# Optimization experiments

Measured on AMD Instinct MI355X. Metric: run time of the kernel, lower is better.

## Reference

```python
import jax, jax.numpy as jnp
import numpy as np

R_MAX = 6.0
NUM_BASIS = 8
TANH_N = 6.0
RECYCLES = 3
N_NODES = 20000
N_EDGES = 640000
ATTR_DIM = 64
LATENT = 64
LN_EPS = 1e-5


def _layer_norm(x, g, b):
    m = x.mean(-1, keepdims=True)
    v = x.var(-1, keepdims=True)
    return (x - m) * jax.lax.rsqrt(v + LN_EPS) * g + b


def setup_inputs() -> dict:
    key = jax.random.key(0)
    ks = jax.random.split(key, 16)
    d1 = 2 * ATTR_DIM + NUM_BASIS  # 136, edge_feature_mlp input
    d2 = LATENT + ATTR_DIM         # 128, attn_mlp input
    d3 = 2 * LATENT                # 128, latent_update_mlp input
    s1 = 1.0 / np.sqrt(d1)
    s2 = 1.0 / np.sqrt(d2)
    s3 = 1.0 / np.sqrt(d3)
    sf = 1.0 / np.sqrt(NUM_BASIS)
    sg = 1.0 / np.sqrt(2 * LATENT)
    return {
        "edge_index": jax.random.randint(ks[0], (2, N_EDGES), 0, N_NODES, dtype=jnp.int64),
        "edge_length": jax.random.uniform(ks[1], (N_EDGES,), minval=0.5, maxval=R_MAX, dtype=jnp.float32),
        "node_attrs": jax.random.normal(ks[2], (N_NODES, ATTR_DIM), dtype=jnp.float32),
        "ln1_g": jnp.ones((d1,), jnp.float32), "ln1_b": jnp.zeros((d1,), jnp.float32),
        "W1": jax.random.normal(ks[3], (d1, LATENT), jnp.float32) * s1,
        "b1": jnp.zeros((LATENT,), jnp.float32),
        "ln2_g": jnp.ones((d2,), jnp.float32), "ln2_b": jnp.zeros((d2,), jnp.float32),
        "W2": jax.random.normal(ks[4], (d2, 1), jnp.float32) * s2,
        "b2": jnp.zeros((1,), jnp.float32),
        "ln3_g": jnp.ones((d3,), jnp.float32), "ln3_b": jnp.zeros((d3,), jnp.float32),
        "W3": jax.random.normal(ks[5], (d3, LATENT), jnp.float32) * s3,
        "b3": jnp.zeros((LATENT,), jnp.float32),
        "film_W1": jax.random.normal(ks[6], (NUM_BASIS, 4 * LATENT), jnp.float32) * sf,  # swiglu: 2*(2*latent)
        "film_W2": jax.random.normal(ks[7], (2 * LATENT, LATENT), jnp.float32) * sg,
        "resnet_p": jnp.zeros((1,), jnp.float32),
    }


def reference(edge_index, edge_length, node_attrs,
              ln1_g, ln1_b, W1, b1,
              ln2_g, ln2_b, W2, b2,
              ln3_g, ln3_b, W3, b3,
              film_W1, film_W2, resnet_p):
    ec = edge_index[0]
    en = edge_index[1]
    num_nodes = node_attrs.shape[0]
    num_edges = edge_index.shape[1]

    # Bessel radial basis * tanh cutoff
    n = jnp.arange(1, NUM_BASIS + 1, dtype=jnp.float32)
    r = edge_length[:, None]
    bessel = jnp.sqrt(2.0 / R_MAX) * jnp.sin(n * jnp.pi * r / R_MAX) / r  # [E, B]
    cutoff = jnp.tanh(1.0 - (edge_length / R_MAX) ** TANH_N) ** 3          # [E]
    rbf = bessel * cutoff[:, None]                                         # [E, B]

    a_c = node_attrs[ec]  # [E, A] gathered center attrs
    a_n = node_attrs[en]  # [E, A] gathered neighbor attrs

    latents = jnp.zeros((num_edges, LATENT), dtype=jnp.float32)
    for _ in range(RECYCLES):  # num_layers=1, recycles=3 -> 3 block applications
        edge_in = jnp.concatenate([a_c, a_n, rbf], axis=-1)            # [E, 136]
        ef = _layer_norm(edge_in, ln1_g, ln1_b) @ W1 + b1              # [E, L]
        attn_in = jnp.concatenate([ef, a_c], axis=-1)                  # [E, 128]
        scores = (_layer_norm(attn_in, ln2_g, ln2_b) @ W2 + b2)[:, 0]  # [E]
        attn = jax.nn.softmax(scores, axis=0)                          # global edge softmax
        pooled = jax.ops.segment_sum(attn[:, None] * ef, ec, num_segments=num_nodes)  # [N, L]
        upd_in = jnp.concatenate([ef, pooled[ec]], axis=-1)            # [E, 2L]
        upd = _layer_norm(upd_in, ln3_g, ln3_b) @ W3 + b3              # [E, L]
        # FiLM gate from rbf: swiglu hidden then sigmoid output, no bias
        h = rbf @ film_W1                                              # [E, 4L]
        a, g = jnp.split(h, 2, axis=-1)
        gate = jax.nn.sigmoid((jax.nn.silu(a) * g) @ film_W2)          # [E, L]
        upd = upd * gate
        uc = jax.nn.sigmoid(resnet_p)                                  # [1]
        c_old = jax.lax.rsqrt(uc * uc + 1.0)
        latents = c_old * latents + (uc * c_old) * upd
    return latents
```

## Files before the change

### kernel.cpp

```cpp
#include <hip/hip_runtime.h>
#include <math.h>

#define KNOTS 1024
#define LNE 1e-5f
#define R0F 0.5f
#define RMAXF 6.0f
#define PAD 96

__device__ __forceinline__ float hermite_(float v0, float m0, float v1, float m1, float t){
  float A = v1 - v0;
  return v0 + t*(m0 + t*((3.f*A - 2.f*m0 - m1) + t*(m0 + m1 - 2.f*A)));
}

__device__ __forceinline__ float wsum64(float v){
#pragma unroll
  for(int m=32;m>=1;m>>=1) v += __shfl_xor(v, m, 64);
  return v;
}

__global__ __launch_bounds__(256) void k_zero(int* cnt, float* sumExp, int N){
  int i = blockIdx.x*256 + threadIdx.x;
  if(i < N) cnt[i] = 0;
  if(i == 0) sumExp[0] = 0.f;
}

__global__ __launch_bounds__(256) void k_weights(
    const float* ln1_g, const float* ln1_b, const float* W1, const float* b1,
    const float* ln2_g, const float* ln2_b, const float* W2, const float* b2,
    const float* ln3_g, const float* ln3_b, const float* W3, const float* b3,
    const float* resnet_p,
    float* W1gA, float* W1gB, float* W1gBot, float* W3gTop, float* W3gBot,
    float* colsum1, float* c1, float* colsum3, float* c3, float* W2g,
    float* cs1w3, float* c1w3, float* BW3, float* misc){
  int tid = threadIdx.x;
  for(int idx=tid; idx<4096; idx+=256){
    int k = idx>>6;
    W1gA[idx]   = ln1_g[k]*W1[idx];
    W1gB[idx]   = ln1_g[64+k]*W1[4096+idx];
    W3gTop[idx] = ln3_g[k]*W3[idx];
    W3gBot[idx] = ln3_g[64+k]*W3[4096+idx];
  }
  for(int idx=tid; idx<512; idx+=256) W1gBot[idx] = ln1_g[128+(idx>>6)]*W1[8192+idx];
  if(tid<128) W2g[tid] = ln2_g[tid]*W2[tid];
  if(tid<64){
    float cs=0.f, cc=0.f;
    for(int k=0;k<136;k++){ float wv = W1[k*64+tid]; cs += ln1_g[k]*wv; cc += ln1_b[k]*wv; }
    colsum1[tid] = cs; c1[tid] = cc + b1[tid];
    float cs3=0.f, cc3=0.f;
    for(int k=0;k<128;k++){ float wv = W3[k*64+tid]; cs3 += ln3_g[k]*wv; cc3 += ln3_b[k]*wv; }
    colsum3[tid] = cs3; c3[tid] = cc3 + b3[tid];
  }
  if(tid==0){
    float cs2=0.f, cc2=0.f;
    for(int k=0;k<128;k++){ cs2 += ln2_g[k]*W2[k]; cc2 += ln2_b[k]*W2[k]; }
    misc[0]=cs2; misc[1]=cc2 + b2[0];
    float p = resnet_p[0];
    float uc = 1.f/(1.f+expf(-p));
    float co = rsqrtf(uc*uc+1.f);
    misc[2] = uc*co*(1.f + co + co*co);
  }
  __syncthreads();
  if(tid<64){
    float a=0.f, b=0.f;
    for(int k=0;k<64;k++){ float wv = W3gTop[k*64+tid]; a += colsum1[k]*wv; b += c1[k]*wv; }
    cs1w3[tid]=a; c1w3[tid]=b;
  }
  for(int idx=tid; idx<512; idx+=256){
    int kk = idx>>6, j = idx&63;
    float a=0.f;
    for(int k=0;k<64;k++) a += W1gBot[kk*64+k]*W3gTop[k*64+j];
    BW3[idx]=a;
  }
  if(tid==0){
    float a=0.f,b=0.f;
    for(int k=0;k<64;k++){ a += colsum1[k]*W2g[k]; b += c1[k]*W2g[k]; }
    misc[3]=a; misc[4]=b;
    float a5=0.f, a6=0.f;
    for(int k=0;k<64;k++){ a5 += colsum1[k]; a6 += c1[k]; }
    misc[5]=a5; misc[6]=a6;
    float gg=0.f, gc=0.f, ccs=0.f;
    for(int k=0;k<64;k++){ float g=colsum1[k], c=c1[k]; gg+=g*g; gc+=g*c; ccs+=c*c; }
    misc[16]=gg; misc[17]=gc; misc[18]=ccs;
  }
  if(tid<8){
    float a=0.f;
    for(int k=0;k<64;k++) a += W1gBot[tid*64+k]*W2g[k];
    misc[8+tid]=a;
  }
}

__device__ __forceinline__ void eval_all(
    float r, const float* W1gBot, const float* BW3, const float* bw2,
    const float* F1, const float* F2, float* uL, int lane, float* rbfO,
    float& T1, float& T13, float& T12, float& gate, float& sr, float& sq){
  float rbf[8];
  float inv_r = 1.f/r;
  float x = r*(1.f/6.f);
  float x2 = x*x;
  float x6 = x2*x2*x2;
  float th = tanhf(1.f - x6);
  float cut = th*th*th;
  float pref = 0.57735026919f*inv_r*cut;
  sr=0.f; sq=0.f;
#pragma unroll
  for(int n=0;n<8;n++){
    float b = pref*sinf((float)(n+1)*0.52359877559f*r);
    rbf[n]=b; rbfO[n]=b; sr+=b; sq+=b*b;
  }
  float t1=0.f,t3=0.f,t2=0.f;
#pragma unroll
  for(int k=0;k<8;k++){
    t1 += rbf[k]*W1gBot[k*64+lane];
    t3 += rbf[k]*BW3[k*64+lane];
    t2 += rbf[k]*bw2[k];
  }
  T1=t1; T13=t3; T12=t2;
  float a0=0.f,a1=0.f,g0=0.f,g1=0.f;
#pragma unroll
  for(int k=0;k<8;k++){
    const float* row = F1 + k*256;
    float rb = rbf[k];
    a0 += rb*row[lane];      a1 += rb*row[64+lane];
    g0 += rb*row[128+lane];  g1 += rb*row[192+lane];
  }
  uL[lane]    = (a0/(1.f+expf(-a0)))*g0;
  uL[64+lane] = (a1/(1.f+expf(-a1)))*g1;
  float accv = 0.f;
  for(int i2=0;i2<128;i2++) accv += uL[i2]*F2[i2*64+lane];
  gate = 1.f/(1.f+expf(-accv));
}

__global__ __launch_bounds__(256) void k_tables(
    const float* W1gBot, const float* BW3, const float* misc,
    const float* F1, const float* F2, const float* colsum1, const float* c1,
    float* tab2, float* tabS, float* tabRbf){
  __shared__ __align__(16) float u[4][128];
  int lane = threadIdx.x&63, w = threadIdx.x>>6;
  int knot = blockIdx.x*4 + w;
  if(knot > KNOTS) return;
  const float H = (RMAXF-R0F)/KNOTS;
  float r = R0F + knot*H;
  const float dh = 1e-3f;
  const float* bw2 = misc+8;
  float rbc[8], rbp[8], rbm[8];
  float T1c,T13c,T12c,Gc,SRc,SQc, T1p,T13p,T12p,Gp,SRp,SQp, T1m,T13m,T12m,Gm,SRm,SQm;
  eval_all(r,    W1gBot,BW3,bw2,F1,F2,u[w],lane, rbc, T1c,T13c,T12c,Gc,SRc,SQc);
  eval_all(r+dh, W1gBot,BW3,bw2,F1,F2,u[w],lane, rbp, T1p,T13p,T12p,Gp,SRp,SQp);
  eval_all(r-dh, W1gBot,BW3,bw2,F1,F2,u[w],lane, rbm, T1m,T13m,T12m,Gm,SRm,SQm);
  float sc = H/(2.f*dh);
  float cg = colsum1[lane], cl = c1[lane];
  float sT1c = wsum64(T1c), sT1p = wsum64(T1p), sT1m = wsum64(T1m);
  float T11c = wsum64(T1c*T1c), T11p = wsum64(T1p*T1p), T11m = wsum64(T1m*T1m);
  float T1gc = wsum64(T1c*cg), T1gp = wsum64(T1p*cg), T1gm = wsum64(T1m*cg);
  float T1cc = wsum64(T1c*cl), T1cp = wsum64(T1p*cl), T1cm = wsum64(T1m*cl);
  ((float4*)tab2)[knot*64+lane] = make_float4(T13c,(T13p-T13m)*sc, Gc,(Gp-Gm)*sc);
  if(lane==0){
    float* d = tabS + knot*16;
    d[0]=SRc;  d[1]=(SRp-SRm)*sc;   d[2]=SQc;  d[3]=(SQp-SQm)*sc;
    d[4]=T12c; d[5]=(T12p-T12m)*sc; d[6]=sT1c; d[7]=(sT1p-sT1m)*sc;
    d[8]=T11c; d[9]=(T11p-T11m)*sc; d[10]=T1gc; d[11]=(T1gp-T1gm)*sc;
    d[12]=T1cc; d[13]=(T1cp-T1cm)*sc; d[14]=0.f; d[15]=0.f;
    float* rb = tabRbf + knot*16;
#pragma unroll
    for(int k=0;k<8;k++){ rb[2*k]=rbc[k]; rb[2*k+1]=(rbp[k]-rbm[k])*sc; }
  }
}

__global__ __launch_bounds__(256) void k_node(
    const float* attrs, const float* W1gA, const float* W1gB, const float* W3gTop,
    const float* W2g, const float* W1gBot, const float* colsum1, const float* c1,
    float* P, float* Q, float* QW3, float* PW3R,
    float* nodeC, float* nodeN, int N){
  __shared__ __align__(16) float sb[4][192];
  int v = (blockIdx.x*256+threadIdx.x)>>6;
  int lane = threadIdx.x&63, w = (threadIdx.x>>6)&3;
  if(v>=N) return;
  const float* av = attrs + (size_t)v*64;
  float al = av[lane];
  sb[w][lane] = al;
  float s = wsum64(al), sqv = wsum64(al*al), t = wsum64(al*W2g[64+lane]);
  float p=0.f, q=0.f;
  const float4* avv = (const float4*)(&sb[w][0]);
#pragma unroll
  for(int kk=0;kk<16;kk++){
    float4 x = avv[kk];
    const float* wa = W1gA + kk*256 + lane;
    const float* wb = W1gB + kk*256 + lane;
    p += x.x*wa[0] + x.y*wa[64] + x.z*wa[128] + x.w*wa[192];
    q += x.x*wb[0] + x.y*wb[64] + x.z*wb[128] + x.w*wb[192];
  }
  P[v*64+lane]=p; Q[v*64+lane]=q;
  float sp = wsum64(p), sq2 = wsum64(q);
  float pw2 = wsum64(p*W2g[lane]), qw2 = wsum64(q*W2g[lane]);
  float cg = colsum1[lane], cl = c1[lane];
  float SPP = wsum64(p*p), SQQ = wsum64(q*q);
  float SPg = wsum64(p*cg), SQg = wsum64(q*cg);
  float SPc = wsum64(p*cl), SQc = wsum64(q*cl);
  float pbv[8], qbv[8];
#pragma unroll
  for(int k=0;k<8;k++){
    float wv = W1gBot[k*64+lane];
    pbv[k] = wsum64(p*wv);
    qbv[k] = wsum64(q*wv);
  }
  sb[w][64+lane]=p; sb[w][128+lane]=q;
  float ap=0.f, aq=0.f;
  const float4* pv = (const float4*)(&sb[w][64]);
  const float4* qv = (const float4*)(&sb[w][128]);
#pragma unroll
  for(int kk=0;kk<16;kk++){
    float4 xp = pv[kk], xq = qv[kk];
    const float* wc = W3gTop + kk*256 + lane;
    ap += xp.x*wc[0] + xp.y*wc[64] + xp.z*wc[128] + xp.w*wc[192];
    aq += xq.x*wc[0] + xq.y*wc[64] + xq.z*wc[128] + xq.w*wc[192];
  }
  PW3R[v*128 + 2*lane] = ap;
  QW3[v*64+lane] = aq;
  if(lane==0){
    float* nc = nodeC + v*16;
    nc[0]=s; nc[1]=sqv; nc[2]=t; nc[3]=pw2; nc[4]=SPP; nc[5]=SPg; nc[6]=SPc; nc[7]=sp;
#pragma unroll
    for(int k=0;k<8;k++) nc[8+k]=pbv[k];
    float* nn = nodeN + v*16;
    nn[0]=s; nn[1]=sqv; nn[2]=sq2; nn[3]=qw2; nn[4]=SQQ; nn[5]=SQg; nn[6]=SQc; nn[7]=0.f;
#pragma unroll
    for(int k=0;k<8;k++) nn[8+k]=qbv[k];
  }
}

__global__ __launch_bounds__(256) void k_bin(const int* ei, const float* elen,
                                             int* cnt, float4* binRec, int N, int E){
  int e = blockIdx.x*256+threadIdx.x;
  if(e<E){
    int c = ei[e]; c = min(max(c,0),N-1);
    int nb = ei[E+e]; nb = min(max(nb,0),N-1);
    float r = elen[e];
    int pos = atomicAdd(&cnt[c],1);
    if(pos < PAD)
      binRec[c*PAD+pos] = make_float4(__int_as_float(nb), r, __int_as_float(e), 0.f);
  }
}

__global__ __launch_bounds__(256) void k_pool(
    const float4* binRec, const int* cnt,
    const float* P, const float* Q,
    const float* nodeC, const float* nodeN, const float* W1gBot,
    const float* colsum1, const float* c1, const float* misc,
    const float* tabS, const float* tabRbf,
    float* pooled, float4* aux, float* sumExp, int N){
  __shared__ float scal[4][PAD][17];
  int w = threadIdx.x>>6, lane = threadIdx.x&63;
  int v = blockIdx.x*4 + w;
  int vv = min(v, N-1);
  int deg = (v<N) ? min(cnt[vv], PAD) : 0;
  const float invH = (float)KNOTS/(RMAXF-R0F);
  int base = vv*PAD;
  {
    float cc0=nodeC[vv*16+0], cc1=nodeC[vv*16+1], cc3=nodeC[vv*16+3];
    float cc4=nodeC[vv*16+4], cc5=nodeC[vv*16+5], cc6=nodeC[vv*16+6], cc7=nodeC[vv*16+7];
    float pb[8];
#pragma unroll
    for(int k=0;k<8;k++) pb[k]=nodeC[vv*16+8+k];
    float csw2=misc[3], cw2=misc[4], sumCol=misc[5], sumC1=misc[6];
    float Sgg=misc[16], Sgc1=misc[17], Sc1c1=misc[18];
    for(int slot=lane; slot<deg; slot+=64){
      float4 rec = binRec[base+slot];
      int nb = __float_as_int(rec.x);
      float r = rec.y;
      float uu = (r-R0F)*invH;
      int ti = (int)uu; ti = min(max(ti,0),KNOTS-1);
      float tt = uu-(float)ti;
      const float4* sA4 = (const float4*)(tabS + ti*16);
      const float4* sB4 = (const float4*)(tabS + (ti+1)*16);
      float4 sA0=sA4[0], sA1=sA4[1], sA2=sA4[2], sA3=sA4[3];
      float4 sB0=sB4[0], sB1=sB4[1], sB2=sB4[2], sB3=sB4[3];
      const float4* rA4 = (const float4*)(tabRbf + ti*16);
      const float4* rB4 = (const float4*)(tabRbf + (ti+1)*16);
      float rbf[8];
      {
        float4 a0=rA4[0], a1=rA4[1], a2=rA4[2], a3=rA4[3];
        float4 b0=rB4[0], b1=rB4[1], b2=rB4[2], b3=rB4[3];
        rbf[0]=hermite_(a0.x,a0.y,b0.x,b0.y,tt); rbf[1]=hermite_(a0.z,a0.w,b0.z,b0.w,tt);
        rbf[2]=hermite_(a1.x,a1.y,b1.x,b1.y,tt); rbf[3]=hermite_(a1.z,a1.w,b1.z,b1.w,tt);
        rbf[4]=hermite_(a2.x,a2.y,b2.x,b2.y,tt); rbf[5]=hermite_(a2.z,a2.w,b2.z,b2.w,tt);
        rbf[6]=hermite_(a3.x,a3.y,b3.x,b3.y,tt); rbf[7]=hermite_(a3.z,a3.w,b3.z,b3.w,tt);
      }
      float srb = hermite_(sA0.x,sA0.y,sB0.x,sB0.y,tt);
      float sqb = hermite_(sA0.z,sA0.w,sB0.z,sB0.w,tt);
      float t1w2= hermite_(sA1.x,sA1.y,sB1.x,sB1.y,tt);
      float sT1 = hermite_(sA1.z,sA1.w,sB1.z,sB1.w,tt);
      float T11 = hermite_(sA2.x,sA2.y,sB2.x,sB2.y,tt);
      float T1g = hermite_(sA2.z,sA2.w,sB2.z,sB2.w,tt);
      float T1c1= hermite_(sA3.x,sA3.y,sB3.x,sB3.y,tt);
      const float4* nn4 = (const float4*)(nodeN + (size_t)nb*16);
      float4 nn0=nn4[0], nn1=nn4[1], nn2=nn4[2], nn3=nn4[3];
      float PT1 = rbf[0]*pb[0]+rbf[1]*pb[1]+rbf[2]*pb[2]+rbf[3]*pb[3]
                + rbf[4]*pb[4]+rbf[5]*pb[5]+rbf[6]*pb[6]+rbf[7]*pb[7];
      float QT1 = rbf[0]*nn2.x+rbf[1]*nn2.y+rbf[2]*nn2.z+rbf[3]*nn2.w
                + rbf[4]*nn3.x+rbf[5]*nn3.y+rbf[6]*nn3.z+rbf[7]*nn3.w;
      float m = (cc0 + nn0.x + srb)*(1.f/136.f);
      float var = (cc1 + nn0.y + sqb)*(1.f/136.f) - m*m;
      float rs = rsqrtf(var + LNE);
      float sumEf = rs*(cc7 + nn0.z + sT1 - m*sumCol) + sumC1;
      float sw = rs*(cc3 + nn0.w + t1w2 - m*csw2) + cw2;
      float SS0 = rs*rs*(cc4 + nn1.x + T11 + 2.f*(PT1+QT1)
                          - 2.f*m*(cc5 + nn1.y + T1g) + m*m*Sgg)
                + 2.f*rs*(cc6 + nn1.z + T1c1 - m*Sgc1) + Sc1c1;
      float* L = &scal[w][slot][0];
      L[0]=rs; L[1]=m; L[2]=sumEf; L[3]=sw; L[4]=SS0; L[5]=2.f*rs*rs;
#pragma unroll
      for(int k=0;k<8;k++) L[6+k]=rbf[k];
    }
  }
  __syncthreads();
  float acc = 0.f, accE = 0.f;
  if(v < N && deg > 0){
    float Pl = P[vv*64+lane];
    float colg1 = colsum1[lane], c1l = c1[lane];
    float w1b[8];
#pragma unroll
    for(int k=0;k<8;k++) w1b[k] = W1gBot[k*64+lane];
    float cc0=nodeC[vv*16+0], cc1=nodeC[vv*16+1], cc2=nodeC[vv*16+2];
    float cs2=misc[0], c2v=misc[1];
    const float inv128 = 1.f/128.f;
    int i1 = min(1, deg-1);
    float4 rA = binRec[base], rB = binRec[base+i1];
    float qA = Q[__float_as_int(rA.x)*64+lane];
    float qB = Q[__float_as_int(rB.x)*64+lane];
    for(int i=0; i<deg; i+=2){
      float4 recA = rA, recB = rB;
      float QlA = qA, QlB = qB;
      bool hasB = (i+1) < deg;
      int iB = min(i+1, deg-1);
      if(i+2 < deg){
        int p0 = i+2, p1 = min(i+3, deg-1);
        rA = binRec[base+p0]; rB = binRec[base+p1];
        qA = Q[__float_as_int(rA.x)*64+lane];
        qB = Q[__float_as_int(rB.x)*64+lane];
      }
      const float* LA = &scal[w][i][0];
      const float* LB = &scal[w][iB][0];
      float rsA=LA[0], mA=LA[1], seA=LA[2], swA=LA[3], S0A=LA[4], cdA=LA[5];
      float rsB=LB[0], mB=LB[1], seB=LB[2], swB=LB[3], S0B=LB[4], cdB=LB[5];
      float T1A = LA[6]*w1b[0]+LA[7]*w1b[1]+LA[8]*w1b[2]+LA[9]*w1b[3]
                + LA[10]*w1b[4]+LA[11]*w1b[5]+LA[12]*w1b[6]+LA[13]*w1b[7];
      float T1B = LB[6]*w1b[0]+LB[7]*w1b[1]+LB[8]*w1b[2]+LB[9]*w1b[3]
                + LB[10]*w1b[4]+LB[11]*w1b[5]+LB[12]*w1b[6]+LB[13]*w1b[7];
      float efA = rsA*(Pl + QlA + T1A - mA*colg1) + c1l;
      float efB = rsB*(Pl + QlB + T1B - mB*colg1) + c1l;
      float dA = Pl*QlA, dB = Pl*QlB;
#pragma unroll
      for(int msk=32; msk>=1; msk>>=1){
        dA += __shfl_xor(dA,msk,64);
        dB += __shfl_xor(dB,msk,64);
      }
      float r1A = S0A + cdA*dA;
      float m2A = (seA + cc0)*inv128;
      float var2A = (r1A + cc1)*inv128 - m2A*m2A;
      float rs2A = rsqrtf(var2A + LNE);
      float scoreA = rs2A*(swA + cc2 - m2A*cs2) + c2v;
      float eevA = __expf(scoreA);
      acc += eevA*efA; accE += eevA;
      if(lane==0) aux[__float_as_int(recA.z)] = make_float4(r1A, rsA, mA, seA);
      if(hasB){
        float r1B = S0B + cdB*dB;
        float m2B = (seB + cc0)*inv128;
        float var2B = (r1B + cc1)*inv128 - m2B*m2B;
        float rs2B = rsqrtf(var2B + LNE);
        float scoreB = rs2B*(swB + cc2 - m2B*cs2) + c2v;
        float eevB = __expf(scoreB);
        acc += eevB*efB; accE += eevB;
        if(lane==0) aux[__float_as_int(recB.z)] = make_float4(r1B, rsB, mB, seB);
      }
    }
  }
  if(v < N){
    pooled[vv*64+lane] = acc;
    if(lane==0 && accE != 0.f) atomicAdd(sumExp, accE);
  }
}

__global__ __launch_bounds__(256) void k_node2(
    const float* pooledRaw, const float* sumExp, const float* W3gBot, const float* nodeC,
    float* PW3R, float4* packF, int N){
  __shared__ __align__(16) float sb[4][64];
  int v = (blockIdx.x*256+threadIdx.x)>>6;
  int lane = threadIdx.x&63, w = (threadIdx.x>>6)&3;
  if(v>=N) return;
  float inv = 1.f/sumExp[0];
  float pl = pooledRaw[v*64+lane]*inv;
  float s = wsum64(pl), sq = wsum64(pl*pl);
  sb[w][lane] = pl;
  float acc = 0.f;
  const float4* pv = (const float4*)(&sb[w][0]);
#pragma unroll
  for(int kk=0;kk<16;kk++){
    float4 x = pv[kk];
    const float* wc = W3gBot + kk*256 + lane;
    acc += x.x*wc[0] + x.y*wc[64] + x.z*wc[128] + x.w*wc[192];
  }
  PW3R[v*128 + 2*lane + 1] = acc;
  if(lane==0){ packF[v] = make_float4(s, sq, nodeC[v*16+7], 0.f); }
}

#define FCHUNK 16
__global__ __launch_bounds__(256) void k_final(
    const int* ei, const float* elen, const float4* aux,
    const float* QW3, const float* PW3R, const float4* packF,
    const float* cs1w3, const float* c1w3, const float* colsum3, const float* c3,
    const float* misc, const float* tab2,
    float* out, int N, int E){
  int w = threadIdx.x>>6, lane = threadIdx.x&63;
  int st = (blockIdx.x*4 + w)*FCHUNK;
  if(st >= E) return;
  int ed = min(st+FCHUNK, E);
  float csw3 = cs1w3[lane], cw3 = c1w3[lane];
  float col3 = colsum3[lane], c3l = c3[lane];
  float SC = misc[2];
  const float invH = (float)KNOTS/(RMAXF-R0F);
  for(int i=st; i<ed; i+=2){
    int eA = i, eB = min(i+1, ed-1);
    int cA = ei[eA];   cA = min(max(cA,0),N-1);
    int nA = ei[E+eA]; nA = min(max(nA,0),N-1);
    int cB = ei[eB];   cB = min(max(cB,0),N-1);
    int nB = ei[E+eB]; nB = min(max(nB,0),N-1);
    float rrA = elen[eA], rrB = elen[eB];
    float4 xA = aux[eA], xB = aux[eB];
    float2 pwA = ((const float2*)PW3R)[cA*64+lane];
    float2 pwB = ((const float2*)PW3R)[cB*64+lane];
    float q3A = QW3[nA*64+lane];
    float q3B = QW3[nB*64+lane];
    float4 pfA = packF[cA], pfB = packF[cB];
    float uuA = (rrA - R0F)*invH;
    int tiA = (int)uuA; tiA = min(max(tiA,0),KNOTS-1);
    float ttA = uuA - (float)tiA;
    int tbA = tiA*64+lane;
    float uuB = (rrB - R0F)*invH;
    int tiB = (int)uuB; tiB = min(max(tiB,0),KNOTS-1);
    float ttB = uuB - (float)tiB;
    int tbB = tiB*64+lane;
    float4 t2aA = ((const float4*)tab2)[tbA], t2bA = ((const float4*)tab2)[tbA+64];
    float4 t2aB = ((const float4*)tab2)[tbB], t2bB = ((const float4*)tab2)[tbB+64];
    {
      float T13 = hermite_(t2aA.x,t2aA.y,t2bA.x,t2bA.y,ttA);
      float gate= hermite_(t2aA.z,t2aA.w,t2bA.z,t2bA.w,ttA);
      float r1 = xA.x, rs = xA.y, m = xA.z, sEf = xA.w;
      float efd = rs*(pwA.x + q3A + T13 - m*csw3) + cw3;
      float m3 = (sEf + pfA.x)*(1.f/128.f);
      float var3 = (r1 + pfA.y)*(1.f/128.f) - m3*m3;
      float rs3 = rsqrtf(var3 + LNE);
      float upd = rs3*(efd + pwA.y - m3*col3) + c3l;
      out[(size_t)eA*64 + lane] = SC*upd*gate;
    }
    {
      float T13 = hermite_(t2aB.x,t2aB.y,t2bB.x,t2bB.y,ttB);
      float gate= hermite_(t2aB.z,t2aB.w,t2bB.z,t2bB.w,ttB);
      float r1 = xB.x, rs = xB.y, m = xB.z, sEf = xB.w;
      float efd = rs*(pwB.x + q3B + T13 - m*csw3) + cw3;
      float m3 = (sEf + pfB.x)*(1.f/128.f);
      float var3 = (r1 + pfB.y)*(1.f/128.f) - m3*m3;
      float rs3 = rsqrtf(var3 + LNE);
      float upd = rs3*(efd + pwB.y - m3*col3) + c3l;
      out[(size_t)eB*64 + lane] = SC*upd*gate;
    }
  }
}

extern "C" void kernel_launch(void* const* d_in, const int* in_sizes, int n_in,
                              void* d_out, int out_size, void* d_ws, size_t ws_size,
                              hipStream_t stream){
  const int*   ei    = (const int*)  d_in[0];
  const float* elen  = (const float*)d_in[1];
  const float* attrs = (const float*)d_in[2];
  const float* ln1_g = (const float*)d_in[3];
  const float* ln1_b = (const float*)d_in[4];
  const float* W1    = (const float*)d_in[5];
  const float* b1    = (const float*)d_in[6];
  const float* ln2_g = (const float*)d_in[7];
  const float* ln2_b = (const float*)d_in[8];
  const float* W2    = (const float*)d_in[9];
  const float* b2    = (const float*)d_in[10];
  const float* ln3_g = (const float*)d_in[11];
  const float* ln3_b = (const float*)d_in[12];
  const float* W3    = (const float*)d_in[13];
  const float* b3    = (const float*)d_in[14];
  const float* F1    = (const float*)d_in[15];
  const float* F2    = (const float*)d_in[16];
  const float* resp  = (const float*)d_in[17];
  const int E = in_sizes[1];
  const int N = in_sizes[2]/64;
  float* ws = (float*)d_ws;
  size_t o = 0;
  auto A = [&](size_t n){ size_t rr = o; o += (n + 63) & ~(size_t)63; return rr; };
  float* P      = ws + A((size_t)N*64);
  float* Q      = ws + A((size_t)N*64);
  float* QW3    = ws + A((size_t)N*64);
  float* PW3R   = ws + A((size_t)N*128);
  float* pooled = ws + A((size_t)N*64);
  float* nodeC  = ws + A((size_t)N*16);
  float* nodeN  = ws + A((size_t)N*16);
  float4* packF = (float4*)(ws + A((size_t)N*4));
  float* W1gA   = ws + A(4096);
  float* W1gB   = ws + A(4096);
  float* W1gBot = ws + A(512);
  float* W3gTop = ws + A(4096);
  float* W3gBot = ws + A(4096);
  float* BW3    = ws + A(512);
  float* colsum1= ws + A(64);
  float* c1     = ws + A(64);
  float* cs1w3  = ws + A(64);
  float* c1w3   = ws + A(64);
  float* colsum3= ws + A(64);
  float* c3     = ws + A(64);
  float* W2g    = ws + A(128);
  float* misc   = ws + A(64);
  float* tab2   = ws + A((size_t)(KNOTS+1)*256);
  float* tabS   = ws + A((size_t)(KNOTS+1)*16);
  float* tabRbf = ws + A((size_t)(KNOTS+1)*16);
  float* sumExp = ws + A(64);
  int* cnt      = (int*)(ws + A((size_t)N));
  float4* binRec= (float4*)(ws + A((size_t)N*PAD*4));
  float4* aux   = (float4*)(ws + A((size_t)E*4));
  (void)ws_size; (void)out_size; (void)n_in;
  float* out = (float*)d_out;

  int nb4 = (N+3)/4;
  k_zero<<<(N+255)/256, 256, 0, stream>>>(cnt, sumExp, N);
  k_weights<<<1,256,0,stream>>>(ln1_g,ln1_b,W1,b1,ln2_g,ln2_b,W2,b2,ln3_g,ln3_b,W3,b3,resp,
      W1gA,W1gB,W1gBot,W3gTop,W3gBot,colsum1,c1,colsum3,c3,W2g,cs1w3,c1w3,BW3,misc);
  k_tables<<<(KNOTS+4)/4, 256, 0, stream>>>(W1gBot,BW3,misc,F1,F2,colsum1,c1,tab2,tabS,tabRbf);
  k_node<<<nb4,256,0,stream>>>(attrs,W1gA,W1gB,W3gTop,W2g,W1gBot,colsum1,c1,P,Q,QW3,PW3R,nodeC,nodeN,N);
  k_bin<<<(E+255)/256,256,0,stream>>>(ei,elen,cnt,binRec,N,E);
  k_pool<<<nb4,256,0,stream>>>(binRec,cnt,P,Q,nodeC,nodeN,W1gBot,colsum1,c1,misc,tabS,tabRbf,pooled,aux,sumExp,N);
  k_node2<<<nb4,256,0,stream>>>(pooled,sumExp,W3gBot,nodeC,PW3R,packF,N);
  {
    int chunks = (E + FCHUNK - 1)/FCHUNK;
    int blocks = (chunks + 3)/4;
    k_final<<<blocks,256,0,stream>>>(ei,elen,aux,QW3,PW3R,packF,cs1w3,c1w3,colsum3,c3,misc,tab2,out,N,E);
  }
}
```

Before: 748.3 us.

## Move attention score computation into per-edge phase and prefetch edge data in final kernel

In k_pool, each lane now computes the full P·Q dot product for its edge from a shared-memory copy of P. It then evaluates the LayerNorm attention score and exp per edge in the first phase, instead of doing a 64-lane shuffle reduction per edge in the serial second loop. The second loop becomes a lean per-edge accumulation over precomputed weights, and the sumExp reduction moves into a wave-level sum. k_final gains software prefetch of edge indices, lengths and aux records for the next pair of edges. The cost is a 64-wide gather of Q per lane in phase one, which adds memory traffic but removes the serialized shuffle chains.

After: 764.1 us. 1.02x slower.

```diff
diff --git a/kernel.cpp b/kernel.cpp
--- a/kernel.cpp
+++ b/kernel.cpp
@@ -248,25 +248,33 @@
     const float* colsum1, const float* c1, const float* misc,
     const float* tabS, const float* tabRbf,
     float* pooled, float4* aux, float* sumExp, int N){
-  __shared__ float scal[4][PAD][17];
+  __shared__ __align__(16) float sP[4][64];
+  __shared__ __align__(16) float scalA[4][PAD][4];
+  __shared__ __align__(16) float scalR[4][PAD][8];
   int w = threadIdx.x>>6, lane = threadIdx.x&63;
   int v = blockIdx.x*4 + w;
   int vv = min(v, N-1);
   int deg = (v<N) ? min(cnt[vv], PAD) : 0;
   const float invH = (float)KNOTS/(RMAXF-R0F);
   int base = vv*PAD;
-  {
-    float cc0=nodeC[vv*16+0], cc1=nodeC[vv*16+1], cc3=nodeC[vv*16+3];
-    float cc4=nodeC[vv*16+4], cc5=nodeC[vv*16+5], cc6=nodeC[vv*16+6], cc7=nodeC[vv*16+7];
+  if(v < N) sP[w][lane] = P[vv*64+lane];
+  __syncthreads();
+  float accE = 0.f;
+  if(v < N){
+    const float* nc = nodeC + vv*16;
+    float cc0=nc[0], cc1=nc[1], cc2=nc[2], cc3=nc[3];
+    float cc4=nc[4], cc5=nc[5], cc6=nc[6], cc7=nc[7];
     float pb[8];
 #pragma unroll
-    for(int k=0;k<8;k++) pb[k]=nodeC[vv*16+8+k];
-    float csw2=misc[3], cw2=misc[4], sumCol=misc[5], sumC1=misc[6];
+    for(int k=0;k<8;k++) pb[k]=nc[8+k];
+    float cs2=misc[0], c2v=misc[1], csw2=misc[3], cw2=misc[4], sumCol=misc[5], sumC1=misc[6];
     float Sgg=misc[16], Sgc1=misc[17], Sc1c1=misc[18];
+    const float4* pp = (const float4*)(&sP[w][0]);
     for(int slot=lane; slot<deg; slot+=64){
       float4 rec = binRec[base+slot];
       int nb = __float_as_int(rec.x);
       float r = rec.y;
+      int orig = __float_as_int(rec.z);
       float uu = (r-R0F)*invH;
       int ti = (int)uu; ti = min(max(ti,0),KNOTS-1);
       float tt = uu-(float)ti;
@@ -294,6 +302,14 @@
       float T1c1= hermite_(sA3.x,sA3.y,sB3.x,sB3.y,tt);
       const float4* nn4 = (const float4*)(nodeN + (size_t)nb*16);
       float4 nn0=nn4[0], nn1=nn4[1], nn2=nn4[2], nn3=nn4[3];
+      const float4* qv4 = (const float4*)(Q + (size_t)nb*64);
+      float dot = 0.f;
+#pragma unroll
+      for(int kk=0;kk<16;kk++){
+        float4 pq = pp[kk];
+        float4 qq = qv4[kk];
+        dot += pq.x*qq.x + pq.y*qq.y + pq.z*qq.z + pq.w*qq.w;
+      }
       float PT1 = rbf[0]*pb[0]+rbf[1]*pb[1]+rbf[2]*pb[2]+rbf[3]*pb[3]
                 + rbf[4]*pb[4]+rbf[5]*pb[5]+rbf[6]*pb[6]+rbf[7]*pb[7];
       float QT1 = rbf[0]*nn2.x+rbf[1]*nn2.y+rbf[2]*nn2.z+rbf[3]*nn2.w
@@ -303,80 +319,50 @@
       float rs = rsqrtf(var + LNE);
       float sumEf = rs*(cc7 + nn0.z + sT1 - m*sumCol) + sumC1;
       float sw = rs*(cc3 + nn0.w + t1w2 - m*csw2) + cw2;
-      float SS0 = rs*rs*(cc4 + nn1.x + T11 + 2.f*(PT1+QT1)
+      float r1 = rs*rs*(cc4 + nn1.x + T11 + 2.f*(PT1+QT1+dot)
                           - 2.f*m*(cc5 + nn1.y + T1g) + m*m*Sgg)
-                + 2.f*rs*(cc6 + nn1.z + T1c1 - m*Sgc1) + Sc1c1;
-      float* L = &scal[w][slot][0];
-      L[0]=rs; L[1]=m; L[2]=sumEf; L[3]=sw; L[4]=SS0; L[5]=2.f*rs*rs;
-#pragma unroll
-      for(int k=0;k<8;k++) L[6+k]=rbf[k];
+               + 2.f*rs*(cc6 + nn1.z + T1c1 - m*Sgc1) + Sc1c1;
+      float m2 = (sumEf + cc0)*(1.f/128.f);
+      float var2 = (r1 + cc1)*(1.f/128.f) - m2*m2;
+      float rs2 = rsqrtf(var2 + LNE);
+      float score = rs2*(sw + cc2 - m2*cs2) + c2v;
+      float eev = __expf(score);
+      accE += eev;
+      aux[orig] = make_float4(r1, rs, m, sumEf);
+      float4* sa = (float4*)&scalA[w][slot][0];
+      *sa = make_float4(eev*rs, eev, m, rec.x);
+      float4* sr4 = (float4*)&scalR[w][slot][0];
+      sr4[0] = make_float4(rbf[0],rbf[1],rbf[2],rbf[3]);
+      sr4[1] = make_float4(rbf[4],rbf[5],rbf[6],rbf[7]);
     }
   }
+  accE = wsum64(accE);
+  if(v < N && lane==0 && accE != 0.f) atomicAdd(sumExp, accE);
   __syncthreads();
-  float acc = 0.f, accE = 0.f;
-  if(v < N && deg > 0){
-    float Pl = P[vv*64+lane];
+  if(v < N){
+    float acc = 0.f;
+    float Pl = sP[w][lane];
     float colg1 = colsum1[lane], c1l = c1[lane];
-    float w1b[8];
-#pragma unroll
-    for(int k=0;k<8;k++) w1b[k] = W1gBot[k*64+lane];
-    float cc0=nodeC[vv*16+0], cc1=nodeC[vv*16+1], cc2=nodeC[vv*16+2];
-    float cs2=misc[0], c2v=misc[1];
-    const float inv128 = 1.f/128.f;
-    int i1 = min(1, deg-1);
-    float4 rA = binRec[base], rB = binRec[base+i1];
-    float qA = Q[__float_as_int(rA.x)*64+lane];
-    float qB = Q[__float_as_int(rB.x)*64+lane];
-    for(int i=0; i<deg; i+=2){
-      float4 recA = rA, recB = rB;
-      float QlA = qA, QlB = qB;
-      bool hasB = (i+1) < deg;
-      int iB = min(i+1, deg-1);
-      if(i+2 < deg){
-        int p0 = i+2, p1 = min(i+3, deg-1);
-        rA = binRec[base+p0]; rB = binRec[base+p1];
-        qA = Q[__float_as_int(rA.x)*64+lane];
-        qB = Q[__float_as_int(rB.x)*64+lane];
-      }
-      const float* LA = &scal[w][i][0];
-      const float* LB = &scal[w][iB][0];
-      float rsA=LA[0], mA=LA[1], seA=LA[2], swA=LA[3], S0A=LA[4], cdA=LA[5];
-      float rsB=LB[0], mB=LB[1], seB=LB[2], swB=LB[3], S0B=LB[4], cdB=LB[5];
-      float T1A = LA[6]*w1b[0]+LA[7]*w1b[1]+LA[8]*w1b[2]+LA[9]*w1b[3]
-                + LA[10]*w1b[4]+LA[11]*w1b[5]+LA[12]*w1b[6]+LA[13]*w1b[7];
-      float T1B = LB[6]*w1b[0]+LB[7]*w1b[1]+LB[8]*w1b[2]+LB[9]*w1b[3]
-                + LB[10]*w1b[4]+LB[11]*w1b[5]+LB[12]*w1b[6]+LB[13]*w1b[7];
-      float efA = rsA*(Pl + QlA + T1A - mA*colg1) + c1l;
-      float efB = rsB*(Pl + QlB + T1B - mB*colg1) + c1l;
-      float dA = Pl*QlA, dB = Pl*QlB;
-#pragma unroll
-      for(int msk=32; msk>=1; msk>>=1){
-        dA += __shfl_xor(dA,msk,64);
-        dB += __shfl_xor(dB,msk,64);
-      }
-      float r1A = S0A + cdA*dA;
-      float m2A = (seA + cc0)*inv128;
-      float var2A = (r1A + cc1)*inv128 - m2A*m2A;
-      float rs2A = rsqrtf(var2A + LNE);
-      float scoreA = rs2A*(swA + cc2 - m2A*cs2) + c2v;
-      float eevA = __expf(scoreA);
-      acc += eevA*efA; accE += eevA;
-      if(lane==0) aux[__float_as_int(recA.z)] = make_float4(r1A, rsA, mA, seA);
-      if(hasB){
-        float r1B = S0B + cdB*dB;
-        float m2B = (seB + cc0)*inv128;
-        float var2B = (r1B + cc1)*inv128 - m2B*m2B;
-        float rs2B = rsqrtf(var2B + LNE);
-        float scoreB = rs2B*(swB + cc2 - m2B*cs2) + c2v;
-        float eevB = __expf(scoreB);
-        acc += eevB*efB; accE += eevB;
-        if(lane==0) aux[__float_as_int(recB.z)] = make_float4(r1B, rsB, mB, seB);
+    float w1b0=W1gBot[lane],      w1b1=W1gBot[64+lane],  w1b2=W1gBot[128+lane], w1b3=W1gBot[192+lane];
+    float w1b4=W1gBot[256+lane],  w1b5=W1gBot[320+lane], w1b6=W1gBot[384+lane], w1b7=W1gBot[448+lane];
+    if(deg > 0){
+      int nb0 = __float_as_int(scalA[w][0][3]);
+      float Qn = Q[(size_t)nb0*64 + lane];
+      for(int i=0; i<deg; i++){
+        float Ql = Qn;
+        if(i+1 < deg){
+          int nbn = __float_as_int(scalA[w][i+1][3]);
+          Qn = Q[(size_t)nbn*64 + lane];
+        }
+        float4 sa = *(const float4*)&scalA[w][i][0];
+        const float4* sr4 = (const float4*)&scalR[w][i][0];
+        float4 r0 = sr4[0], r1 = sr4[1];
+        float t1 = r0.x*w1b0 + r0.y*w1b1 + r0.z*w1b2 + r0.w*w1b3
+                 + r1.x*w1b4 + r1.y*w1b5 + r1.z*w1b6 + r1.w*w1b7;
+        acc += sa.x*(Pl + Ql + t1 - sa.z*colg1) + sa.y*c1l;
       }
     }
-  }
-  if(v < N){
     pooled[vv*64+lane] = acc;
-    if(lane==0 && accE != 0.f) atomicAdd(sumExp, accE);
   }
 }
 
@@ -418,24 +404,33 @@
   float col3 = colsum3[lane], c3l = c3[lane];
   float SC = misc[2];
   const float invH = (float)KNOTS/(RMAXF-R0F);
+  int cA = min(max(ei[st],0),N-1),      nA = min(max(ei[E+st],0),N-1);
+  int e1 = min(st+1, ed-1);
+  int cB = min(max(ei[e1],0),N-1),      nB = min(max(ei[E+e1],0),N-1);
+  float rrA = elen[st], rrB = elen[e1];
+  float4 xA = aux[st], xB = aux[e1];
   for(int i=st; i<ed; i+=2){
     int eA = i, eB = min(i+1, ed-1);
-    int cA = ei[eA];   cA = min(max(cA,0),N-1);
-    int nA = ei[E+eA]; nA = min(max(nA,0),N-1);
-    int cB = ei[eB];   cB = min(max(cB,0),N-1);
-    int nB = ei[E+eB]; nB = min(max(nB,0),N-1);
-    float rrA = elen[eA], rrB = elen[eB];
-    float4 xA = aux[eA], xB = aux[eB];
-    float2 pwA = ((const float2*)PW3R)[cA*64+lane];
-    float2 pwB = ((const float2*)PW3R)[cB*64+lane];
-    float q3A = QW3[nA*64+lane];
-    float q3B = QW3[nB*64+lane];
-    float4 pfA = packF[cA], pfB = packF[cB];
-    float uuA = (rrA - R0F)*invH;
+    int cAc=cA, nAc=nA, cBc=cB, nBc=nB;
+    float rAc=rrA, rBc=rrB;
+    float4 xAc=xA, xBc=xB;
+    if(i+2 < ed){
+      int p0=i+2, p1=min(i+3, ed-1);
+      cA = min(max(ei[p0],0),N-1); nA = min(max(ei[E+p0],0),N-1);
+      cB = min(max(ei[p1],0),N-1); nB = min(max(ei[E+p1],0),N-1);
+      rrA = elen[p0]; rrB = elen[p1];
+      xA = aux[p0]; xB = aux[p1];
+    }
+    float2 pwA = ((const float2*)PW3R)[cAc*64+lane];
+    float2 pwB = ((const float2*)PW3R)[cBc*64+lane];
+    float q3A = QW3[nAc*64+lane];
+    float q3B = QW3[nBc*64+lane];
+    float4 pfA = packF[cAc], pfB = packF[cBc];
+    float uuA = (rAc - R0F)*invH;
     int tiA = (int)uuA; tiA = min(max(tiA,0),KNOTS-1);
     float ttA = uuA - (float)tiA;
     int tbA = tiA*64+lane;
-    float uuB = (rrB - R0F)*invH;
+    float uuB = (rBc - R0F)*invH;
     int tiB = (int)uuB; tiB = min(max(tiB,0),KNOTS-1);
     float ttB = uuB - (float)tiB;
     int tbB = tiB*64+lane;
@@ -444,7 +439,7 @@
     {
       float T13 = hermite_(t2aA.x,t2aA.y,t2bA.x,t2bA.y,ttA);
       float gate= hermite_(t2aA.z,t2aA.w,t2bA.z,t2bA.w,ttA);
-      float r1 = xA.x, rs = xA.y, m = xA.z, sEf = xA.w;
+      float r1 = xAc.x, rs = xAc.y, m = xAc.z, sEf = xAc.w;
       float efd = rs*(pwA.x + q3A + T13 - m*csw3) + cw3;
       float m3 = (sEf + pfA.x)*(1.f/128.f);
       float var3 = (r1 + pfA.y)*(1.f/128.f) - m3*m3;
@@ -455,7 +450,7 @@
     {
       float T13 = hermite_(t2aB.x,t2aB.y,t2bB.x,t2bB.y,ttB);
       float gate= hermite_(t2aB.z,t2aB.w,t2bB.z,t2bB.w,ttB);
-      float r1 = xB.x, rs = xB.y, m = xB.z, sEf = xB.w;
+      float r1 = xBc.x, rs = xBc.y, m = xBc.z, sEf = xBc.w;
       float efd = rs*(pwB.x + q3B + T13 - m*csw3) + cw3;
       float m3 = (sEf + pfB.x)*(1.f/128.f);
       float var3 = (r1 + pfB.y)*(1.f/128.f) - m3*m3;
```
